# Kernel optimization log

Measured on AMD Instinct MI355X. Metric: run time of the kernel, lower is better.

## Reference

```python
import jax, jax.numpy as jnp
import numpy as np
from jax import lax

D = 256      # key/query dim
D_F = 256    # diff feature channels
C_TOK = 1    # leading context tokens in query_vit
EPS = 1e-6


def conv2d(x, w, b, pad):
    out = lax.conv_general_dilated(x, w, (1, 1), [(pad, pad), (pad, pad)],
                                   dimension_numbers=('NCHW', 'OIHW', 'NCHW'))
    return out + b[None, :, None, None]


def gn1(x, g, b):
    # GroupNorm with 1 group: normalize over (C,H,W) per sample
    mu = jnp.mean(x, axis=(1, 2, 3), keepdims=True)
    var = jnp.var(x, axis=(1, 2, 3), keepdims=True)
    xn = (x - mu) * lax.rsqrt(var + EPS)
    return xn * g[None, :, None, None] + b[None, :, None, None]


def resize_bilinear_ac(x, Ho, Wo):
    # F.interpolate(mode='bilinear', align_corners=True)
    B, C, H, W = x.shape
    ys = jnp.linspace(0.0, H - 1.0, Ho)
    xs = jnp.linspace(0.0, W - 1.0, Wo)
    y0 = jnp.floor(ys).astype(jnp.int32)
    y1 = jnp.minimum(y0 + 1, H - 1)
    wy = (ys - y0)[None, None, :, None]
    x0 = jnp.floor(xs).astype(jnp.int32)
    x1 = jnp.minimum(x0 + 1, W - 1)
    wx = (xs - x0)[None, None, None, :]
    r = x[:, :, y0, :] * (1.0 - wy) + x[:, :, y1, :] * wy
    return r[:, :, :, x0] * (1.0 - wx) + r[:, :, :, x1] * wx


def setup_inputs() -> dict:
    key = jax.random.key(0)
    ks = jax.random.split(key, 12)
    B, Hd, Wd, Ht, Wt = 8, 64, 64, 32, 32

    def kaiming(k, shape, fan_in):
        return jax.random.normal(k, shape, jnp.float32) * np.sqrt(2.0 / fan_in)

    return {
        'query_vit': jax.random.normal(ks[0], (B, C_TOK + Ht * Wt, D), jnp.float32),
        'feat_diff_cat': jax.random.normal(ks[1], (B, 5 * D_F, Hd, Wd), jnp.float32),
        'rb_w1': kaiming(ks[2], (D_F, 5 * D_F, 3, 3), 5 * D_F * 9), 'rb_b1': jnp.zeros((D_F,), jnp.float32),
        'rb_w2': kaiming(ks[3], (D_F, D_F, 3, 3), D_F * 9), 'rb_b2': jnp.zeros((D_F,), jnp.float32),
        'rb_ws': kaiming(ks[4], (D_F, 5 * D_F, 1, 1), 5 * D_F), 'rb_bs': jnp.zeros((D_F,), jnp.float32),
        'ln_g': jnp.ones((D_F,), jnp.float32), 'ln_b': jnp.zeros((D_F,), jnp.float32),
        'key_w': kaiming(ks[5], (D, D_F, 1, 1), D_F), 'key_b': jnp.zeros((D,), jnp.float32),
        'val_w': kaiming(ks[6], (D_F, D_F, 1, 1), D_F), 'val_b': jnp.zeros((D_F,), jnp.float32),
        'dh0_w': kaiming(ks[7], (D_F, D_F, 3, 3), D_F * 9), 'dh0_b': jnp.zeros((D_F,), jnp.float32),
        'dh1_w': kaiming(ks[8], (D_F, D_F, 3, 3), D_F * 9), 'dh1_b': jnp.zeros((D_F,), jnp.float32),
    }


def reference(query_vit, feat_diff_cat, rb_w1, rb_b1, rb_w2, rb_b2, rb_ws, rb_bs,
              ln_g, ln_b, key_w, key_b, val_w, val_b, dh0_w, dh0_b, dh1_w, dh1_b):
    B, _, h_diff, w_diff = feat_diff_cat.shape
    N = query_vit.shape[1] - C_TOK
    h_trm = w_trm = int(N ** 0.5)

    # ResBlock_ysh(D_f*5 -> D_f): conv3x3 + relu + conv3x3, 1x1-projected residual
    h = jax.nn.relu(conv2d(feat_diff_cat, rb_w1, rb_b1, 1))
    h = conv2d(h, rb_w2, rb_b2, 1)
    feat_diff = jax.nn.relu(h + conv2d(feat_diff_cat, rb_ws, rb_bs, 0))

    fln = gn1(feat_diff, ln_g, ln_b)
    key_diff = conv2d(fln, key_w, key_b, 0).reshape(B, D, -1)          # (B, D, HW)
    value_diff = conv2d(fln, val_w, val_b, 0).reshape(B, D_F, -1)      # (B, Df, HW)
    value_diff = jnp.transpose(value_diff, (0, 2, 1))                  # (B, HW, Df)

    # cross attention: (B, C+N, D) @ (B, D, HW) -> softmax -> @ (B, HW, Df)
    scores = jnp.einsum('bnd,bdm->bnm', query_vit, key_diff) * (D ** -0.5)
    attn = jax.nn.softmax(scores, axis=-1)
    out_cross = jnp.einsum('bnm,bmf->bnf', attn, value_diff)           # (B, C+N, Df)

    out_cross_c = out_cross[:, :C_TOK, :]
    out_p = jnp.transpose(out_cross[:, C_TOK:, :], (0, 2, 1)).reshape(B, D_F, h_trm, w_trm)
    out_p = jax.nn.relu(conv2d(out_p, dh0_w, dh0_b, 1))
    out_p = resize_bilinear_ac(out_p, h_diff, w_diff)
    out_p = out_p + feat_diff                                          # DropPath(0) = identity
    out_p = jax.nn.relu(conv2d(gn1(out_p, ln_g, ln_b), dh1_w, dh1_b, 1)) + out_p
    return out_cross_c, out_p
```

## Files before the change

kernel.cpp:

```cpp
#include <hip/hip_runtime.h>
#include <cstdint>
#include <cstddef>

typedef __attribute__((ext_vector_type(4))) float     f32x4;
typedef __attribute__((ext_vector_type(8))) __bf16    bf16x8;
typedef __attribute__((ext_vector_type(8))) short     short8;
typedef __attribute__((ext_vector_type(4))) unsigned short u16x4;
typedef unsigned short u16;

__device__ __forceinline__ float b2f(u16 u) {
  unsigned x = ((unsigned)u) << 16;
  float f;
  __builtin_memcpy(&f, &x, 4);
  return f;
}
__device__ __forceinline__ u16 f2b(float f) {
  unsigned u;
  __builtin_memcpy(&u, &f, 4);
  return (u16)((u + 0x7FFFu + ((u >> 16) & 1u)) >> 16);
}

struct GP {
  const u16*  A;
  const u16*  B;
  const float* bias;
  const void* aux;
  void*       C;
  float*      out0;
  long long   aBS, bBS, cBS, auxBS;
  int Ktot, Mrows, ldc;
  int cin, logW, wpad, poff;
  float scale;
};

#define GLDS16(g, l)                                                        \
  __builtin_amdgcn_global_load_lds(                                         \
      (const void __attribute__((address_space(1)))*)(g),                   \
      (void __attribute__((address_space(3)))*)(l), 16, 0, 0)

struct G256 {
  const u16* A;
  const u16* B;
  float* P;
  long long aBS;
  int Ktot, cin, logW, wpad, poff;
};

__global__ __launch_bounds__(512, 2) void k_gemm256(G256 gp) {
  const int tid = threadIdx.x;
  const int l = tid & 63, w = tid >> 6;
  const int lr = l & 15, lc = l >> 4;
  const int mt = blockIdx.x, sp = blockIdx.y, b = blockIdx.z;
  const int m0 = mt << 8;
  const int wm = w >> 2, wn = w & 3;

  __shared__ __align__(16) u16 sm[2][32768];
  u16* smb = &sm[0][0];

  f32x4 acc[8][4];
#pragma unroll
  for (int i = 0; i < 8; ++i)
#pragma unroll
    for (int j = 0; j < 4; ++j) acc[i][j] = (f32x4){0.f, 0.f, 0.f, 0.f};

  const u16* Ab = gp.A + (size_t)b * gp.aBS;
  const int slot = l & 3;
  const u16* aS[2];
  const u16* bS[2];
#pragma unroll
  for (int j = 0; j < 2; ++j) {
    const int r = j * 128 + w * 16 + (l >> 2);
    const int p = m0 + r;
    const int y = p >> gp.logW, x = p & ((1 << gp.logW) - 1);
    const int sw = (slot ^ ((r >> 1) & 3)) << 3;
    aS[j] = Ab + (size_t)((y + gp.poff) * gp.wpad + (x + gp.poff)) * gp.cin + sw;
    bS[j] = gp.B + (size_t)r * gp.Ktot + sw;
  }
  auto dstA = [&](int buf, int ks, int j) -> u16* {
    return smb + buf * 32768 + ks * 8192 + (j * 128 + w * 16) * 32 + l * 8;
  };
  auto dstB = [&](int buf, int ks, int j) -> u16* {
    return smb + buf * 32768 + 16384 + ks * 8192 + (j * 128 + w * 16) * 32 + l * 8;
  };

  const int Thalf = (gp.Ktot >> 6) >> 1;
  const int kt0 = sp * Thalf;
  int off = kt0 << 6;
  int tap = off / gp.cin;
  int kcS = off - tap * gp.cin;
  int dxS = tap % 3;
  int tapS = (tap / 3) * gp.wpad + dxS;
  int ktS = kt0;

  auto adv = [&](int& kA, int& kB) {
    kB = ktS << 6;
    kA = tapS * gp.cin + kcS;
    kcS += 64;
    if (kcS == gp.cin) {
      kcS = 0; ++dxS; ++tapS;
      if (dxS == 3) { dxS = 0; tapS += gp.wpad - 3; }
    }
    ++ktS;
  };

  {
    int kA, kB;
    adv(kA, kB);
    GLDS16(aS[0] + kA, dstA(0, 0, 0));
    GLDS16(aS[1] + kA, dstA(0, 0, 1));
    GLDS16(bS[0] + kB, dstB(0, 0, 0));
    GLDS16(bS[1] + kB, dstB(0, 0, 1));
    GLDS16(aS[0] + kA + 32, dstA(0, 1, 0));
    GLDS16(aS[1] + kA + 32, dstA(0, 1, 1));
    GLDS16(bS[0] + kB + 32, dstB(0, 1, 0));
    GLDS16(bS[1] + kB + 32, dstB(0, 1, 1));
  }
  asm volatile("s_waitcnt vmcnt(0)" ::: "memory");
  __builtin_amdgcn_s_barrier();

  const int NT = Thalf;
  for (int t = 0; t < NT; ++t) {
    const int buf = t & 1;
    const char* base = (const char*)smb + buf * 65536;
    const bool pf = (t + 1 < NT);
    if (pf) {
      int kA, kB;
      adv(kA, kB);
      GLDS16(aS[0] + kA, dstA(buf ^ 1, 0, 0));
      GLDS16(aS[1] + kA, dstA(buf ^ 1, 0, 1));
      GLDS16(bS[0] + kB, dstB(buf ^ 1, 0, 0));
      GLDS16(bS[1] + kB, dstB(buf ^ 1, 0, 1));
      GLDS16(aS[0] + kA + 32, dstA(buf ^ 1, 1, 0));
      GLDS16(aS[1] + kA + 32, dstA(buf ^ 1, 1, 1));
      GLDS16(bS[0] + kB + 32, dstB(buf ^ 1, 1, 0));
      GLDS16(bS[1] + kB + 32, dstB(buf ^ 1, 1, 1));
    }
    bf16x8 bv0[4], bv1[4];
#pragma unroll
    for (int ni = 0; ni < 4; ++ni) {
      const int row = wn * 64 + ni * 16 + lr;
      const int sw = (lc ^ ((row >> 1) & 3)) << 4;
      bv0[ni] = *(const bf16x8*)(base + 32768 + row * 64 + sw);
      bv1[ni] = *(const bf16x8*)(base + 49152 + row * 64 + sw);
    }
#pragma unroll
    for (int mq = 0; mq < 2; ++mq) {
      bf16x8 a0[4], a1[4];
#pragma unroll
      for (int mi = 0; mi < 4; ++mi) {
        const int row = wm * 128 + (mq * 4 + mi) * 16 + lr;
        const int sw = (lc ^ ((row >> 1) & 3)) << 4;
        a0[mi] = *(const bf16x8*)(base + row * 64 + sw);
        a1[mi] = *(const bf16x8*)(base + 16384 + row * 64 + sw);
      }
#pragma unroll
      for (int mi = 0; mi < 4; ++mi)
#pragma unroll
        for (int ni = 0; ni < 4; ++ni)
          acc[mq * 4 + mi][ni] = __builtin_amdgcn_mfma_f32_16x16x32_bf16(
              a0[mi], bv0[ni], acc[mq * 4 + mi][ni], 0, 0, 0);
#pragma unroll
      for (int mi = 0; mi < 4; ++mi)
#pragma unroll
        for (int ni = 0; ni < 4; ++ni)
          acc[mq * 4 + mi][ni] = __builtin_amdgcn_mfma_f32_16x16x32_bf16(
              a1[mi], bv1[ni], acc[mq * 4 + mi][ni], 0, 0, 0);
    }
    asm volatile("s_waitcnt vmcnt(0)" ::: "memory");
    __builtin_amdgcn_s_barrier();
  }

  float* P = gp.P + ((size_t)sp * 128 + b * 16 + mt) * 65536;
#pragma unroll
  for (int mi = 0; mi < 8; ++mi)
#pragma unroll
    for (int ni = 0; ni < 4; ++ni) {
      const int ncol = wn * 64 + ni * 16 + lr;
      const int mloc = wm * 128 + mi * 16 + lc * 4;
#pragma unroll
      for (int r = 0; r < 4; ++r)
        P[(size_t)(mloc + r) * 256 + ncol] = acc[mi][ni][r];
    }
}

__global__ __launch_bounds__(256) void k_reduceH1(const float* __restrict__ P,
                                                  const float* __restrict__ bias,
                                                  u16* __restrict__ o) {
  const int i4 = blockIdx.x * 256 + threadIdx.x;
  const int flat = i4 << 2;
  const int n0 = flat & 255;
  const int mloc = (flat >> 8) & 255;
  const int gm = flat >> 16;
  const f32x4 a = *(const f32x4*)(P + (size_t)gm * 65536 + mloc * 256 + n0);
  const f32x4 c = *(const f32x4*)(P + (size_t)(128 + gm) * 65536 + mloc * 256 + n0);
  const f32x4 bb = *(const f32x4*)(bias + n0);
  const int batch = gm >> 4;
  const int mg = (gm & 15) * 256 + mloc;
  const int y = mg >> 6, x = mg & 63;
  u16x4 r;
#pragma unroll
  for (int k = 0; k < 4; ++k) r[k] = f2b(fmaxf(a[k] + c[k] + bb[k], 0.f));
  *(u16x4*)(o + ((size_t)batch * 4356 + (size_t)(y + 1) * 66 + x + 1) * 256 + n0) = r;
}

template <int AMODE, int CW, bool RELU>
__global__ __launch_bounds__(512, 2) void k_gemm8(GP gp) {
  const int tid = threadIdx.x;
  const int l = tid & 63, w = tid >> 6;
  const int b = blockIdx.z;
  const int m0 = blockIdx.x * 128;
  const int wm = w >> 2, wn = w & 3;
  const int lr = l & 15, lc = l >> 4;

  __shared__ __align__(16) u16 sm[2][24576];

  f32x4 acc[4][4];
#pragma unroll
  for (int i = 0; i < 4; ++i)
#pragma unroll
    for (int j = 0; j < 4; ++j) acc[i][j] = (f32x4){0.f, 0.f, 0.f, 0.f};

  const u16* Ab = gp.A + (size_t)b * gp.aBS;
  const u16* Bb = gp.B + (size_t)b * gp.bBS;
  const int scoff = (((tid & 7) ^ ((tid >> 3) & 7)) << 3);

  const u16* aP[2];
  const u16* bP[4];
#pragma unroll
  for (int i = 0; i < 2; ++i) {
    const int p = m0 + i * 64 + (tid >> 3);
    if (AMODE == 0) {
      const int pc = p < gp.Mrows ? p : gp.Mrows - 1;
      aP[i] = Ab + (size_t)pc * gp.Ktot + scoff;
    } else {
      const int y = p >> gp.logW, x = p & ((1 << gp.logW) - 1);
      aP[i] = Ab + (size_t)((y + gp.poff) * gp.wpad + (x + gp.poff)) * gp.cin +
              scoff;
    }
  }
#pragma unroll
  for (int i = 0; i < 4; ++i)
    bP[i] = Bb + (size_t)(i * 64 + (tid >> 3)) * gp.Ktot + scoff;

  const int NT = gp.Ktot >> 6;
  int kcS = 0, tapS = 0, dxS = 0, ktS = 0;

  auto adv = [&](int& kA, int& kB) {
    kB = ktS << 6;
    if (AMODE == 0) {
      kA = ktS << 6;
    } else {
      kA = tapS * gp.cin + kcS;
      kcS += 64;
      if (kcS == gp.cin) {
        kcS = 0; ++dxS; ++tapS;
        if (dxS == 3) { dxS = 0; tapS += gp.wpad - 3; }
      }
    }
    ++ktS;
  };

  {
    int kA, kB;
    adv(kA, kB);
    u16* sA = &sm[0][0] + (w << 9);
    u16* sB = &sm[0][8192] + (w << 9);
    GLDS16(aP[0] + kA, sA);
    GLDS16(aP[1] + kA, sA + 4096);
    GLDS16(bP[0] + kB, sB);
    GLDS16(bP[1] + kB, sB + 4096);
    GLDS16(bP[2] + kB, sB + 8192);
    GLDS16(bP[3] + kB, sB + 12288);
  }
  asm volatile("s_waitcnt vmcnt(0)" ::: "memory");
  __builtin_amdgcn_s_barrier();

  for (int t = 0; t < NT; ++t) {
    const int buf = t & 1;
    const u16* sAc = &sm[buf][0];
    const u16* sBc = &sm[buf][8192];
    const bool pf = (t + 1 < NT);
    if (pf) {
      int kA, kB;
      adv(kA, kB);
      u16* sA = &sm[buf ^ 1][0] + (w << 9);
      u16* sB = &sm[buf ^ 1][8192] + (w << 9);
      GLDS16(aP[0] + kA, sA);
      GLDS16(aP[1] + kA, sA + 4096);
      GLDS16(bP[0] + kB, sB);
      GLDS16(bP[1] + kB, sB + 4096);
      GLDS16(bP[2] + kB, sB + 8192);
      GLDS16(bP[3] + kB, sB + 12288);
    }
    bf16x8 av0[4], av1[4], bv0[4], bv1[4];
#pragma unroll
    for (int mi = 0; mi < 4; ++mi) {
      const int row = wm * 64 + mi * 16 + lr;
      av0[mi] = *(const bf16x8*)(sAc + row * 64 + (((0 + lc) ^ (row & 7)) << 3));
      av1[mi] = *(const bf16x8*)(sAc + row * 64 + (((4 + lc) ^ (row & 7)) << 3));
    }
#pragma unroll
    for (int ni = 0; ni < 4; ++ni) {
      const int row = wn * 64 + ni * 16 + lr;
      bv0[ni] = *(const bf16x8*)(sBc + row * 64 + (((0 + lc) ^ (row & 7)) << 3));
      bv1[ni] = *(const bf16x8*)(sBc + row * 64 + (((4 + lc) ^ (row & 7)) << 3));
    }
#pragma unroll
    for (int mi = 0; mi < 4; ++mi)
#pragma unroll
      for (int ni = 0; ni < 4; ++ni)
        acc[mi][ni] = __builtin_amdgcn_mfma_f32_16x16x32_bf16(
            av0[mi], bv0[ni], acc[mi][ni], 0, 0, 0);
#pragma unroll
    for (int mi = 0; mi < 4; ++mi)
#pragma unroll
      for (int ni = 0; ni < 4; ++ni)
        acc[mi][ni] = __builtin_amdgcn_mfma_f32_16x16x32_bf16(
            av1[mi], bv1[ni], acc[mi][ni], 0, 0, 0);
    asm volatile("s_waitcnt vmcnt(0)" ::: "memory");
    __builtin_amdgcn_s_barrier();
  }

#pragma unroll
  for (int mi = 0; mi < 4; ++mi) {
#pragma unroll
    for (int ni = 0; ni < 4; ++ni) {
      const int ncol = wn * 64 + ni * 16 + lr;
      const int mbase = m0 + wm * 64 + mi * 16 + lc * 4;
      const float bv_ = gp.bias ? gp.bias[ncol] : 0.f;
      if constexpr (CW == 0) {
#pragma unroll
        for (int r = 0; r < 4; ++r) {
          float v = acc[mi][ni][r] + bv_;
          if (RELU) v = fmaxf(v, 0.f);
          ((u16*)gp.C)[(size_t)b * gp.cBS + (size_t)(mbase + r) * 256 + ncol] =
              f2b(v);
        }
      } else if constexpr (CW == 1) {
#pragma unroll
        for (int r = 0; r < 4; ++r) {
          float v = acc[mi][ni][r] + bv_;
          if (RELU) v = fmaxf(v, 0.f);
          const int mrow = mbase + r;
          const int y = mrow >> 6, x = mrow & 63;
          ((u16*)gp.C)[(size_t)b * gp.cBS +
                       (size_t)((y + 1) * 66 + x + 1) * 256 + ncol] = f2b(v);
        }
      } else if constexpr (CW == 2) {
#pragma unroll
        for (int r = 0; r < 4; ++r) {
          const int mrow = mbase + r;
          const float s =
              b2f(((const u16*)gp.aux)[(size_t)b * gp.auxBS +
                                       (size_t)mrow * 256 + ncol]);
          float v = acc[mi][ni][r] + bv_ + s;
          v = fmaxf(v, 0.f);
          ((float*)gp.C)[(size_t)b * gp.cBS + (size_t)mrow * 256 + ncol] = v;
        }
      } else if constexpr (CW == 6) {
        float* Cf =
            (float*)gp.C + (size_t)b * gp.cBS + (size_t)ncol * 4096 + mbase;
        const float* mid = (const float*)gp.aux + (size_t)b * gp.auxBS;
        f32x4 o;
#pragma unroll
        for (int r = 0; r < 4; ++r) {
          float v = acc[mi][ni][r] + bv_;
          v = fmaxf(v, 0.f);
          o[r] = v + mid[(size_t)(mbase + r) * 256 + ncol];
        }
        *(f32x4*)Cf = o;
      }
    }
  }
}

template <int AMODE, int CW, bool RELU>
__global__ __launch_bounds__(256, 2) void k_gemm(GP gp) {
  const int tid = threadIdx.x;
  const int l = tid & 63, w = tid >> 6;
  const int b = blockIdx.z;
  const int m0 = blockIdx.x * 128, n0 = blockIdx.y * 128;
  const int wm = w >> 1, wn = w & 1;

  __shared__ __align__(16) u16 smA[128 * 64];
  __shared__ __align__(16) u16 smB[128 * 64];

  f32x4 acc[4][4];
#pragma unroll
  for (int i = 0; i < 4; ++i)
#pragma unroll
    for (int j = 0; j < 4; ++j) acc[i][j] = (f32x4){0.f, 0.f, 0.f, 0.f};

  const u16* Ab = gp.A + (size_t)b * gp.aBS;
  const u16* Bb = gp.B + (size_t)b * gp.bBS;

  const int scoff = (((l & 7) ^ (l >> 3)) << 3);

  const u16* aRow[4];
  const u16* bRow[4];
  u16* ldsA[4];
  u16* ldsB[4];
#pragma unroll
  for (int i = 0; i < 4; ++i) {
    const int r = w * 32 + i * 8 + (l >> 3);
    bRow[i] = Bb + (size_t)(n0 + r) * gp.Ktot + scoff;
    const int p = m0 + r;
    if (AMODE == 0) {
      const int pc = p < gp.Mrows ? p : gp.Mrows - 1;
      aRow[i] = Ab + (size_t)pc * gp.Ktot + scoff;
    } else {
      const int y = p >> gp.logW, x = p & ((1 << gp.logW) - 1);
      const int icoord = (y + gp.poff) * gp.wpad + (x + gp.poff);
      aRow[i] = Ab + (size_t)icoord * gp.cin + scoff;
    }
    ldsA[i] = smA + (w * 32 + i * 8) * 64;
    ldsB[i] = smB + (w * 32 + i * 8) * 64;
  }

  const int ktiles = gp.Ktot >> 6;
  int tap_off = 0, dx = 0, kc = 0;

  for (int kt = 0; kt < ktiles; ++kt) {
    int koffA;
    if (AMODE == 0)
      koffA = kt << 6;
    else
      koffA = tap_off * gp.cin + kc;
    const int koffB = kt << 6;
#pragma unroll
    for (int i = 0; i < 4; ++i) GLDS16(aRow[i] + koffA, ldsA[i]);
#pragma unroll
    for (int i = 0; i < 4; ++i) GLDS16(bRow[i] + koffB, ldsB[i]);

    if (AMODE == 1) {
      kc += 64;
      if (kc == gp.cin) {
        kc = 0;
        ++dx;
        ++tap_off;
        if (dx == 3) { dx = 0; tap_off += gp.wpad - 3; }
      }
    }

    __syncthreads();
#pragma unroll
    for (int ks = 0; ks < 2; ++ks) {
      bf16x8 av[4], bv[4];
      const int cc = (ks << 2) + (l >> 4);
#pragma unroll
      for (int mi = 0; mi < 4; ++mi) {
        const int row = wm * 64 + mi * 16 + (l & 15);
        av[mi] = *(const bf16x8*)((const char*)smA + (row << 7) +
                                  ((cc ^ (row & 7)) << 4));
      }
#pragma unroll
      for (int ni = 0; ni < 4; ++ni) {
        const int row = wn * 64 + ni * 16 + (l & 15);
        bv[ni] = *(const bf16x8*)((const char*)smB + (row << 7) +
                                  ((cc ^ (row & 7)) << 4));
      }
#pragma unroll
      for (int mi = 0; mi < 4; ++mi)
#pragma unroll
        for (int ni = 0; ni < 4; ++ni)
          acc[mi][ni] = __builtin_amdgcn_mfma_f32_16x16x32_bf16(
              av[mi], bv[ni], acc[mi][ni], 0, 0, 0);
    }
    __syncthreads();
  }

#pragma unroll
  for (int mi = 0; mi < 4; ++mi) {
#pragma unroll
    for (int ni = 0; ni < 4; ++ni) {
      const int ncol = n0 + wn * 64 + ni * 16 + (l & 15);
      const int mbase = m0 + wm * 64 + mi * 16 + ((l >> 4) << 2);
      const float bv_ = gp.bias ? gp.bias[ncol] : 0.f;

      if constexpr (CW == 3) {
        u16* Cu = (u16*)gp.C + (size_t)b * gp.cBS + (size_t)ncol * 4096 + mbase;
        u16x4 pk;
#pragma unroll
        for (int r = 0; r < 4; ++r) pk[r] = f2b(acc[mi][ni][r] + bv_);
        *(u16x4*)Cu = pk;
      } else if constexpr (CW == 7) {
        u16* base = (u16*)gp.C;
        if (ncol < 256) {
#pragma unroll
          for (int r = 0; r < 4; ++r)
            base[(size_t)b * 1048576 + (size_t)(mbase + r) * 256 + ncol] =
                f2b(acc[mi][ni][r] + bv_);
        } else {
          u16x4 pk;
#pragma unroll
          for (int r = 0; r < 4; ++r) pk[r] = f2b(acc[mi][ni][r] + bv_);
          *(u16x4*)(base + 8388608 + (size_t)b * 1048576 +
                    (size_t)(ncol - 256) * 4096 + mbase) = pk;
        }
      } else {
#pragma unroll
        for (int reg = 0; reg < 4; ++reg) {
          const int mrow = mbase + reg;
          if (mrow >= gp.Mrows) continue;
          float v = acc[mi][ni][reg] * gp.scale + bv_;
          if (RELU) v = v > 0.f ? v : 0.f;
          if constexpr (CW == 0) {
            ((u16*)gp.C)[(size_t)b * gp.cBS + (size_t)mrow * gp.ldc + ncol] =
                f2b(v);
          } else if constexpr (CW == 4) {
            if (mrow == 0) {
              gp.out0[(size_t)b * 256 + ncol] = v;
            } else {
              const int p = mrow - 1, y = p >> 5, x = p & 31;
              ((u16*)gp.C)[(size_t)b * gp.cBS +
                           (size_t)((y + 1) * 34 + (x + 1)) * 256 + ncol] =
                  f2b(v);
            }
          } else if constexpr (CW == 5) {
            ((float*)gp.C)[(size_t)b * gp.cBS + (size_t)mrow * 256 + ncol] = v;
          }
        }
      }
    }
  }
}


__global__ __launch_bounds__(256) void k_prep_x(const float* __restrict__ x,
                                                u16* __restrict__ o) {
  __shared__ float t[32][65];
  const int b = blockIdx.z, c0 = blockIdx.y << 5, y = blockIdx.x;
  const float* src = x + ((size_t)b * 1280 + c0) * 4096 + (size_t)y * 64;
#pragma unroll
  for (int i = 0; i < 8; ++i) {
    const int idx = threadIdx.x + (i << 8);
    const int c = idx >> 6, xx = idx & 63;
    t[c][xx] = src[(size_t)c * 4096 + xx];
  }
  __syncthreads();
  u16* dst = o + ((size_t)b * 4356 + (size_t)(y + 1) * 66 + 1) * 1280 + c0;
#pragma unroll
  for (int i = 0; i < 8; ++i) {
    const int idx = threadIdx.x + (i << 8);
    const int xx = idx >> 5, c = idx & 31;
    dst[(size_t)xx * 1280 + c] = f2b(t[c][xx]);
  }
}

__global__ __launch_bounds__(256) void k_zero_border(u16* __restrict__ p,
                                                     int P, int C) {
  const int per_img = (4 * P - 4) * C;
  const int total = 8 * per_img;
  for (int idx = blockIdx.x * 256 + threadIdx.x; idx < total;
       idx += gridDim.x * 256) {
    const int b = idx / per_img;
    const int r = idx % per_img;
    const int pix = r / C, c = r % C;
    int y, x;
    const int Pm = P - 1;
    if (pix < P) { y = 0; x = pix; }
    else if (pix < 2 * P) { y = Pm; x = pix - P; }
    else if (pix < 3 * P - 2) { y = pix - 2 * P + 1; x = 0; }
    else { y = pix - (3 * P - 2) + 1; x = Pm; }
    p[((size_t)b * P * P + (size_t)y * P + x) * C + c] = 0;
  }
}

__global__ __launch_bounds__(256) void k_prep_w3(const float* __restrict__ w,
                                                 u16* __restrict__ o, int cin,
                                                 int n) {
  for (int i = blockIdx.x * 256 + threadIdx.x; i < n; i += gridDim.x * 256) {
    const int ci = i % cin;
    const int r = i / cin;
    const int t = r % 9;
    const int co = r / 9;
    o[i] = f2b(w[((size_t)co * cin + ci) * 9 + t]);
  }
}

__global__ __launch_bounds__(256) void k_f2b(const float* __restrict__ x,
                                             u16* __restrict__ o, int n) {
  for (int i = blockIdx.x * 256 + threadIdx.x; i < n; i += gridDim.x * 256)
    o[i] = f2b(x[i]);
}

__global__ __launch_bounds__(256) void k_gn_stats(const float* __restrict__ x,
                                                  float* __restrict__ st) {
  const int b = blockIdx.y;
  const f32x4* xb = (const f32x4*)(x + (size_t)b * 1048576);
  float s = 0.f, s2 = 0.f;
  for (int i = blockIdx.x * 256 + threadIdx.x; i < 262144;
       i += gridDim.x * 256) {
    const f32x4 v = xb[i];
    s += v[0] + v[1] + v[2] + v[3];
    s2 += v[0] * v[0] + v[1] * v[1] + v[2] * v[2] + v[3] * v[3];
  }
#pragma unroll
  for (int o = 32; o; o >>= 1) {
    s += __shfl_down(s, o);
    s2 += __shfl_down(s2, o);
  }
  __shared__ float ls[4], ls2[4];
  const int w = threadIdx.x >> 6;
  if ((threadIdx.x & 63) == 0) { ls[w] = s; ls2[w] = s2; }
  __syncthreads();
  if (threadIdx.x == 0) {
    atomicAdd(&st[b * 2], ls[0] + ls[1] + ls[2] + ls[3]);
    atomicAdd(&st[b * 2 + 1], ls2[0] + ls2[1] + ls2[2] + ls2[3]);
  }
}

template <bool PAD>
__global__ __launch_bounds__(256) void k_gn_norm(const float* __restrict__ x,
                                                 const float* __restrict__ st,
                                                 const float* __restrict__ g,
                                                 const float* __restrict__ bb,
                                                 u16* __restrict__ o) {
  const int b = blockIdx.y;
  const float mu = st[b * 2] * (1.f / 1048576.f);
  const float var = st[b * 2 + 1] * (1.f / 1048576.f) - mu * mu;
  const float rs = rsqrtf(var + 1e-6f);
  const int i4 = blockIdx.x * 256 + threadIdx.x;
  const f32x4 v = ((const f32x4*)(x + (size_t)b * 1048576))[i4];
  const int flat = i4 << 2;
  const int c = flat & 255;
  const int p = flat >> 8;
  const f32x4 gv = *(const f32x4*)(g + c);
  const f32x4 bv = *(const f32x4*)(bb + c);
  u16x4 r;
#pragma unroll
  for (int k = 0; k < 4; ++k) r[k] = f2b((v[k] - mu) * rs * gv[k] + bv[k]);
  size_t oidx;
  if (PAD) {
    const int y = p >> 6, xx = p & 63;
    oidx = ((size_t)b * 4356 + (size_t)(y + 1) * 66 + xx + 1) * 256 + c;
  } else {
    oidx = ((size_t)b * 4096 + p) * 256 + c;
  }
  *(u16x4*)(o + oidx) = r;
}

__global__ __launch_bounds__(256) void k_softmax(u16* __restrict__ s) {
  const size_t row = blockIdx.x;
  u16* p = s + row * 4096;
  const int t = threadIdx.x;
  const short8 r0 = ((const short8*)p)[t];
  const short8 r1 = ((const short8*)p)[t + 256];
  float v[16];
#pragma unroll
  for (int i = 0; i < 8; ++i) {
    v[i] = b2f((u16)r0[i]);
    v[8 + i] = b2f((u16)r1[i]);
  }
  float m = v[0];
#pragma unroll
  for (int i = 1; i < 16; ++i) m = fmaxf(m, v[i]);
#pragma unroll
  for (int o = 32; o; o >>= 1) m = fmaxf(m, __shfl_xor(m, o));
  __shared__ float lm[4], lsum[4];
  const int w = t >> 6;
  if ((t & 63) == 0) lm[w] = m;
  __syncthreads();
  m = fmaxf(fmaxf(lm[0], lm[1]), fmaxf(lm[2], lm[3]));
  float sum = 0.f;
#pragma unroll
  for (int i = 0; i < 16; ++i) {
    v[i] = __expf(v[i] - m);
    sum += v[i];
  }
#pragma unroll
  for (int o = 32; o; o >>= 1) sum += __shfl_xor(sum, o);
  if ((t & 63) == 0) lsum[w] = sum;
  __syncthreads();
  sum = lsum[0] + lsum[1] + lsum[2] + lsum[3];
  const float inv = 1.f / sum;
  short8 o0, o1;
#pragma unroll
  for (int i = 0; i < 8; ++i) {
    o0[i] = (short)f2b(v[i] * inv);
    o1[i] = (short)f2b(v[8 + i] * inv);
  }
  ((short8*)p)[t] = o0;
  ((short8*)p)[t + 256] = o1;
}

__global__ __launch_bounds__(256) void k_resize_add(const float* __restrict__ d0,
                                                    const float* __restrict__ F,
                                                    float* __restrict__ mid) {
  const int i4 = blockIdx.x * 256 + threadIdx.x;
  const int flat = i4 << 2;
  const int c = flat & 255;
  const int p = (flat >> 8) & 4095;
  const int b = flat >> 20;
  const int y = p >> 6, x = p & 63;
  const float fy = y * (31.f / 63.f);
  const int y0 = (int)fy;
  const float wy = fy - y0;
  const int y1 = y0 + 1 > 31 ? 31 : y0 + 1;
  const float fx = x * (31.f / 63.f);
  const int x0 = (int)fx;
  const float wx = fx - x0;
  const int x1 = x0 + 1 > 31 ? 31 : x0 + 1;
  const float* db = d0 + (size_t)b * 262144;
  const f32x4 a = *(const f32x4*)(db + ((size_t)(y0 * 32 + x0) << 8) + c);
  const f32x4 bq = *(const f32x4*)(db + ((size_t)(y0 * 32 + x1) << 8) + c);
  const f32x4 cq = *(const f32x4*)(db + ((size_t)(y1 * 32 + x0) << 8) + c);
  const f32x4 dq = *(const f32x4*)(db + ((size_t)(y1 * 32 + x1) << 8) + c);
  f32x4 r = (a * (1.f - wx) + bq * wx) * (1.f - wy) +
            (cq * (1.f - wx) + dq * wx) * wy;
  r += *(const f32x4*)(F + (size_t)flat);
  *(f32x4*)(mid + (size_t)flat) = r;
}


extern "C" void kernel_launch(void* const* d_in, const int* in_sizes, int n_in,
                              void* d_out, int out_size, void* d_ws,
                              size_t ws_size, hipStream_t stream) {
  (void)in_sizes; (void)n_in; (void)out_size;

  const float* q   = (const float*)d_in[0];
  const float* xdc = (const float*)d_in[1];
  const float* w1  = (const float*)d_in[2];
  const float* b1  = (const float*)d_in[3];
  const float* w2  = (const float*)d_in[4];
  const float* b2  = (const float*)d_in[5];
  const float* wsc = (const float*)d_in[6];
  const float* bsc = (const float*)d_in[7];
  const float* lng = (const float*)d_in[8];
  const float* lnb = (const float*)d_in[9];
  const float* wk  = (const float*)d_in[10];
  const float* bk  = (const float*)d_in[11];
  const float* wv  = (const float*)d_in[12];
  const float* bv  = (const float*)d_in[13];
  const float* wd0 = (const float*)d_in[14];
  const float* bd0 = (const float*)d_in[15];
  const float* wd1 = (const float*)d_in[16];
  const float* bd1 = (const float*)d_in[17];

  char* ws = (char*)d_ws;
  size_t cur = 0;
  auto alloc = [&](size_t sz) {
    char* p = ws + cur;
    cur += sz;
    return p;
  };
  u16* XPAD = (u16*)alloc(89194496);
  u16* W1R  = (u16*)alloc(5898240);
  u16* W2R  = (u16*)alloc(1179648);
  u16* WSR  = (u16*)alloc(655360);
  u16* WKV  = (u16*)alloc(262144);
  float* BKV = (float*)alloc(2048);
  u16* WD0R = (u16*)alloc(1179648);
  u16* WD1R = (u16*)alloc(1179648);
  u16* SB   = (u16*)alloc(16777216);
  u16* H1   = (u16*)alloc(17842176);
  float* F  = (float*)alloc(33554432);
  u16* FLN  = (u16*)alloc(16777216);
  u16* KT   = (u16*)alloc(16777216);
  u16* V    = (u16*)alloc(16777216);
  u16* QB   = (u16*)alloc(4198400);
  u16* OCP  = (u16*)alloc(4734976);
  float* D0O = (float*)alloc(8388608);
  float* MID = (float*)alloc(33554432);
  u16* G2   = (u16*)alloc(17842176);
  float* ST = (float*)alloc(256);
  u16* SCORES = XPAD;
  float* PART = (float*)FLN;
  (void)V;

  if (ws_size < cur) return;

  float* out0 = (float*)d_out;
  float* out1 = (float*)d_out + 2048;

  hipMemsetAsync(ST, 0, 256, stream);
  hipMemcpyAsync(BKV, bk, 1024, hipMemcpyDeviceToDevice, stream);
  hipMemcpyAsync(BKV + 256, bv, 1024, hipMemcpyDeviceToDevice, stream);

  k_zero_border<<<2048, 256, 0, stream>>>(XPAD, 66, 1280);
  k_zero_border<<<1024, 256, 0, stream>>>(H1, 66, 256);
  k_zero_border<<<1024, 256, 0, stream>>>(G2, 66, 256);

  k_prep_x<<<dim3(64, 40, 8), 256, 0, stream>>>(xdc, XPAD);
  k_prep_w3<<<2048, 256, 0, stream>>>(w1, W1R, 1280, 2949120);
  k_prep_w3<<<1024, 256, 0, stream>>>(w2, W2R, 256, 589824);
  k_prep_w3<<<1024, 256, 0, stream>>>(wd0, WD0R, 256, 589824);
  k_prep_w3<<<1024, 256, 0, stream>>>(wd1, WD1R, 256, 589824);
  k_f2b<<<512, 256, 0, stream>>>(wsc, WSR, 327680);
  k_f2b<<<128, 256, 0, stream>>>(wk, WKV, 65536);
  k_f2b<<<128, 256, 0, stream>>>(wv, WKV + 65536, 65536);

  const dim3 g8(32, 1, 8);
  {
    GP g{};
    g.A = XPAD; g.B = WSR; g.bias = bsc; g.C = SB;
    g.aBS = 5575680; g.bBS = 0; g.cBS = 1048576;
    g.Ktot = 1280; g.Mrows = 4096; g.ldc = 256;
    g.cin = 1280; g.logW = 6; g.wpad = 66; g.poff = 1; g.scale = 1.f;
    k_gemm8<1, 0, false><<<g8, 512, 0, stream>>>(g);
  }
  {
    G256 g{};
    g.A = XPAD; g.B = W1R; g.P = PART;
    g.aBS = 5575680; g.Ktot = 11520;
    g.cin = 1280; g.logW = 6; g.wpad = 66; g.poff = 0;
    k_gemm256<<<dim3(16, 2, 8), 512, 0, stream>>>(g);
    k_reduceH1<<<8192, 256, 0, stream>>>(PART, b1, H1);
  }
  k_f2b<<<2048, 256, 0, stream>>>(q, QB, 2099200);
  k_zero_border<<<512, 256, 0, stream>>>(OCP, 34, 256);

  {
    GP g{};
    g.A = H1; g.B = W2R; g.bias = b2; g.C = F; g.aux = SB;
    g.aBS = 1115136; g.bBS = 0; g.cBS = 1048576; g.auxBS = 1048576;
    g.Ktot = 2304; g.Mrows = 4096; g.ldc = 256;
    g.cin = 256; g.logW = 6; g.wpad = 66; g.poff = 0; g.scale = 1.f;
    k_gemm8<1, 2, false><<<g8, 512, 0, stream>>>(g);
  }
  k_gn_stats<<<dim3(64, 8), 256, 0, stream>>>(F, ST);
  k_gn_norm<false><<<dim3(1024, 8), 256, 0, stream>>>(F, ST, lng, lnb, FLN);
  {
    GP g{};
    g.A = FLN; g.B = WKV; g.bias = BKV; g.C = KT;
    g.aBS = 1048576; g.bBS = 0; g.cBS = 0;
    g.Ktot = 256; g.Mrows = 4096; g.ldc = 256; g.scale = 1.f;
    k_gemm<0, 7, false><<<dim3(32, 4, 8), 256, 0, stream>>>(g);
  }
  {
    GP g{};
    g.A = QB; g.B = KT; g.bias = nullptr; g.C = SCORES;
    g.aBS = 262400; g.bBS = 1048576; g.cBS = 4198400;
    g.Ktot = 256; g.Mrows = 1025; g.ldc = 4096; g.scale = 0.0625f;
    k_gemm<0, 0, false><<<dim3(9, 32, 8), 256, 0, stream>>>(g);
  }
  k_softmax<<<8200, 256, 0, stream>>>(SCORES);
  {
    GP g{};
    g.A = SCORES; g.B = V; g.bias = nullptr; g.C = OCP; g.out0 = out0;
    g.aBS = 4198400; g.bBS = 1048576; g.cBS = 295936;
    g.Ktot = 4096; g.Mrows = 1025; g.ldc = 256; g.scale = 1.f;
    k_gemm<0, 4, false><<<dim3(9, 2, 8), 256, 0, stream>>>(g);
  }
  {
    GP g{};
    g.A = OCP; g.B = WD0R; g.bias = bd0; g.C = D0O;
    g.aBS = 295936; g.bBS = 0; g.cBS = 262144;
    g.Ktot = 2304; g.Mrows = 1024; g.ldc = 256;
    g.cin = 256; g.logW = 5; g.wpad = 34; g.poff = 0; g.scale = 1.f;
    k_gemm<1, 5, true><<<dim3(8, 2, 8), 256, 0, stream>>>(g);
  }
  k_resize_add<<<8192, 256, 0, stream>>>(D0O, F, MID);
  k_gn_stats<<<dim3(64, 8), 256, 0, stream>>>(MID, ST + 16);
  k_gn_norm<true><<<dim3(1024, 8), 256, 0, stream>>>(MID, ST + 16, lng, lnb, G2);
  {
    GP g{};
    g.A = G2; g.B = WD1R; g.bias = bd1; g.C = out1; g.aux = MID;
    g.aBS = 1115136; g.bBS = 0; g.cBS = 1048576; g.auxBS = 1048576;
    g.Ktot = 2304; g.Mrows = 4096; g.ldc = 256;
    g.cin = 256; g.logW = 6; g.wpad = 66; g.poff = 0; g.scale = 1.f;
    k_gemm8<1, 6, false><<<g8, 512, 0, stream>>>(g);
  }
}
```

Measured before the change: 730.7 us.

## Fuse shortcut conv into conv2 GEMM, fold GroupNorm into K/V weights, merge prep kernels

The 1x1 shortcut conv is concatenated along K into the second 3x3 conv GEMM, so one GEMM reads H1 and the padded input and writes F in both fp32 and bf16. That GEMM's epilogue also accumulates the GroupNorm statistics with atomics. The first GroupNorm is then folded into per-batch key/value weights and biases by a small kernel, which removes the separate stats, normalize and FLN passes. The query scale moves into the query conversion, the second GroupNorm's stats move into the resize-add kernel, and the border-zeroing and weight-prep launches are merged into single kernels. In exchange, statistics come from atomics with a single-pass variance, and the folded per-batch weights are quantized to bf16 after scaling, which can change accuracy.

```diff
diff --git a/kernel.cpp b/kernel.cpp
--- a/kernel.cpp
+++ b/kernel.cpp
@@ -27,7 +27,8 @@
   const void* aux;
   void*       C;
   float*      out0;
-  long long   aBS, bBS, cBS, auxBS;
+  float*      st;
+  long long   aBS, bBS, cBS, auxBS, biasBS;
   int Ktot, Mrows, ldc;
   int cin, logW, wpad, poff;
   float scale;
@@ -203,7 +204,7 @@
   *(u16x4*)(o + ((size_t)batch * 4356 + (size_t)(y + 1) * 66 + x + 1) * 256 + n0) = r;
 }
 
-template <int AMODE, int CW, bool RELU>
+template <int AMODE, int CW>
 __global__ __launch_bounds__(512, 2) void k_gemm8(GP gp) {
   const int tid = threadIdx.x;
   const int l = tid & 63, w = tid >> 6;
@@ -225,53 +226,52 @@
   const int scoff = (((tid & 7) ^ ((tid >> 3) & 7)) << 3);
 
   const u16* aP[2];
-  const u16* bP[4];
+  const u16* aP2[2];
 #pragma unroll
   for (int i = 0; i < 2; ++i) {
     const int p = m0 + i * 64 + (tid >> 3);
-    if (AMODE == 0) {
-      const int pc = p < gp.Mrows ? p : gp.Mrows - 1;
-      aP[i] = Ab + (size_t)pc * gp.Ktot + scoff;
-    } else {
-      const int y = p >> gp.logW, x = p & ((1 << gp.logW) - 1);
-      aP[i] = Ab + (size_t)((y + gp.poff) * gp.wpad + (x + gp.poff)) * gp.cin +
-              scoff;
-    }
-  }
+    const int y = p >> 6, x = p & 63;
+    aP[i] = Ab + (size_t)(y * 66 + x) * gp.cin + scoff;
+    if (AMODE == 2) {
+      const u16* Xb = (const u16*)gp.aux + (size_t)b * gp.auxBS;
+      aP2[i] = Xb + (size_t)((y + 1) * 66 + (x + 1)) * 1280 + scoff;
+    }
+  }
+  const u16* bP[4];
 #pragma unroll
   for (int i = 0; i < 4; ++i)
     bP[i] = Bb + (size_t)(i * 64 + (tid >> 3)) * gp.Ktot + scoff;
 
   const int NT = gp.Ktot >> 6;
-  int kcS = 0, tapS = 0, dxS = 0, ktS = 0;
-
-  auto adv = [&](int& kA, int& kB) {
-    kB = ktS << 6;
-    if (AMODE == 0) {
-      kA = ktS << 6;
+  const int seg1t = (AMODE == 2) ? 36 : 0x7fffffff;
+  int kcS = 0, tapS = 0, dxS = 0, nstg = 0;
+
+  auto stage = [&](int buf) {
+    const int kt = nstg++;
+    const int kB = kt << 6;
+    u16* sA = &sm[buf][0] + (w << 9);
+    u16* sB = &sm[buf][8192] + (w << 9);
+    if (AMODE == 2 && kt >= seg1t) {
+      const int kA = (kt - seg1t) << 6;
+      GLDS16(aP2[0] + kA, sA);
+      GLDS16(aP2[1] + kA, sA + 4096);
     } else {
-      kA = tapS * gp.cin + kcS;
+      const int kA = tapS * gp.cin + kcS;
       kcS += 64;
       if (kcS == gp.cin) {
         kcS = 0; ++dxS; ++tapS;
-        if (dxS == 3) { dxS = 0; tapS += gp.wpad - 3; }
+        if (dxS == 3) { dxS = 0; tapS += 63; }
       }
-    }
-    ++ktS;
-  };
-
-  {
-    int kA, kB;
-    adv(kA, kB);
-    u16* sA = &sm[0][0] + (w << 9);
-    u16* sB = &sm[0][8192] + (w << 9);
-    GLDS16(aP[0] + kA, sA);
-    GLDS16(aP[1] + kA, sA + 4096);
+      GLDS16(aP[0] + kA, sA);
+      GLDS16(aP[1] + kA, sA + 4096);
+    }
     GLDS16(bP[0] + kB, sB);
     GLDS16(bP[1] + kB, sB + 4096);
     GLDS16(bP[2] + kB, sB + 8192);
     GLDS16(bP[3] + kB, sB + 12288);
-  }
+  };
+
+  stage(0);
   asm volatile("s_waitcnt vmcnt(0)" ::: "memory");
   __builtin_amdgcn_s_barrier();
 
@@ -279,19 +279,8 @@
     const int buf = t & 1;
     const u16* sAc = &sm[buf][0];
     const u16* sBc = &sm[buf][8192];
-    const bool pf = (t + 1 < NT);
-    if (pf) {
-      int kA, kB;
-      adv(kA, kB);
-      u16* sA = &sm[buf ^ 1][0] + (w << 9);
-      u16* sB = &sm[buf ^ 1][8192] + (w << 9);
-      GLDS16(aP[0] + kA, sA);
-      GLDS16(aP[1] + kA, sA + 4096);
-      GLDS16(bP[0] + kB, sB);
-      GLDS16(bP[1] + kB, sB + 4096);
-      GLDS16(bP[2] + kB, sB + 8192);
-      GLDS16(bP[3] + kB, sB + 12288);
-    }
+    if (t + 1 < NT) stage(buf ^ 1);
+
     bf16x8 av0[4], av1[4], bv0[4], bv1[4];
 #pragma unroll
     for (int mi = 0; mi < 4; ++mi) {
@@ -321,55 +310,56 @@
     __builtin_amdgcn_s_barrier();
   }
 
+  float lsum = 0.f, lsq = 0.f;
 #pragma unroll
   for (int mi = 0; mi < 4; ++mi) {
 #pragma unroll
     for (int ni = 0; ni < 4; ++ni) {
       const int ncol = wn * 64 + ni * 16 + lr;
       const int mbase = m0 + wm * 64 + mi * 16 + lc * 4;
-      const float bv_ = gp.bias ? gp.bias[ncol] : 0.f;
-      if constexpr (CW == 0) {
+      const float bv_ = gp.bias[ncol];
+      if constexpr (CW == 8) {
+        float* F = (float*)gp.C + (size_t)b * gp.cBS;
+        u16* FB = (u16*)gp.out0 + (size_t)b * gp.cBS;
 #pragma unroll
         for (int r = 0; r < 4; ++r) {
-          float v = acc[mi][ni][r] + bv_;
-          if (RELU) v = fmaxf(v, 0.f);
-          ((u16*)gp.C)[(size_t)b * gp.cBS + (size_t)(mbase + r) * 256 + ncol] =
-              f2b(v);
+          float v = fmaxf(acc[mi][ni][r] + bv_, 0.f);
+          const size_t idx = (size_t)(mbase + r) * 256 + ncol;
+          F[idx] = v;
+          FB[idx] = f2b(v);
+          lsum += v;
+          lsq += v * v;
         }
-      } else if constexpr (CW == 1) {
-#pragma unroll
-        for (int r = 0; r < 4; ++r) {
-          float v = acc[mi][ni][r] + bv_;
-          if (RELU) v = fmaxf(v, 0.f);
-          const int mrow = mbase + r;
-          const int y = mrow >> 6, x = mrow & 63;
-          ((u16*)gp.C)[(size_t)b * gp.cBS +
-                       (size_t)((y + 1) * 66 + x + 1) * 256 + ncol] = f2b(v);
-        }
-      } else if constexpr (CW == 2) {
-#pragma unroll
-        for (int r = 0; r < 4; ++r) {
-          const int mrow = mbase + r;
-          const float s =
-              b2f(((const u16*)gp.aux)[(size_t)b * gp.auxBS +
-                                       (size_t)mrow * 256 + ncol]);
-          float v = acc[mi][ni][r] + bv_ + s;
-          v = fmaxf(v, 0.f);
-          ((float*)gp.C)[(size_t)b * gp.cBS + (size_t)mrow * 256 + ncol] = v;
-        }
-      } else if constexpr (CW == 6) {
+      } else {
         float* Cf =
             (float*)gp.C + (size_t)b * gp.cBS + (size_t)ncol * 4096 + mbase;
         const float* mid = (const float*)gp.aux + (size_t)b * gp.auxBS;
         f32x4 o;
 #pragma unroll
         for (int r = 0; r < 4; ++r) {
-          float v = acc[mi][ni][r] + bv_;
-          v = fmaxf(v, 0.f);
+          float v = fmaxf(acc[mi][ni][r] + bv_, 0.f);
           o[r] = v + mid[(size_t)(mbase + r) * 256 + ncol];
         }
         *(f32x4*)Cf = o;
       }
+    }
+  }
+  if constexpr (CW == 8) {
+    __syncthreads();
+#pragma unroll
+    for (int o = 32; o; o >>= 1) {
+      lsum += __shfl_down(lsum, o);
+      lsq += __shfl_down(lsq, o);
+    }
+    float* red = (float*)&sm[0][0];
+    if (l == 0) { red[w * 2] = lsum; red[w * 2 + 1] = lsq; }
+    __syncthreads();
+    if (tid == 0) {
+      float s = 0.f, s2 = 0.f;
+#pragma unroll
+      for (int k = 0; k < 8; ++k) { s += red[k * 2]; s2 += red[k * 2 + 1]; }
+      atomicAdd(&gp.st[b * 2], s);
+      atomicAdd(&gp.st[b * 2 + 1], s2);
     }
   }
 }
@@ -475,15 +465,10 @@
     for (int ni = 0; ni < 4; ++ni) {
       const int ncol = n0 + wn * 64 + ni * 16 + (l & 15);
       const int mbase = m0 + wm * 64 + mi * 16 + ((l >> 4) << 2);
-      const float bv_ = gp.bias ? gp.bias[ncol] : 0.f;
-
-      if constexpr (CW == 3) {
-        u16* Cu = (u16*)gp.C + (size_t)b * gp.cBS + (size_t)ncol * 4096 + mbase;
-        u16x4 pk;
-#pragma unroll
-        for (int r = 0; r < 4; ++r) pk[r] = f2b(acc[mi][ni][r] + bv_);
-        *(u16x4*)Cu = pk;
-      } else if constexpr (CW == 7) {
+      const float bv_ =
+          gp.bias ? gp.bias[(size_t)b * gp.biasBS + ncol] : 0.f;
+
+      if constexpr (CW == 7) {
         u16* base = (u16*)gp.C;
         if (ncol < 256) {
 #pragma unroll
@@ -547,67 +532,98 @@
   }
 }
 
-__global__ __launch_bounds__(256) void k_zero_border(u16* __restrict__ p,
-                                                     int P, int C) {
+__device__ __forceinline__ void zb1(u16* p, int P, int C, int idx) {
   const int per_img = (4 * P - 4) * C;
-  const int total = 8 * per_img;
-  for (int idx = blockIdx.x * 256 + threadIdx.x; idx < total;
-       idx += gridDim.x * 256) {
-    const int b = idx / per_img;
-    const int r = idx % per_img;
-    const int pix = r / C, c = r % C;
-    int y, x;
-    const int Pm = P - 1;
-    if (pix < P) { y = 0; x = pix; }
-    else if (pix < 2 * P) { y = Pm; x = pix - P; }
-    else if (pix < 3 * P - 2) { y = pix - 2 * P + 1; x = 0; }
-    else { y = pix - (3 * P - 2) + 1; x = Pm; }
-    p[((size_t)b * P * P + (size_t)y * P + x) * C + c] = 0;
-  }
-}
-
-__global__ __launch_bounds__(256) void k_prep_w3(const float* __restrict__ w,
-                                                 u16* __restrict__ o, int cin,
-                                                 int n) {
-  for (int i = blockIdx.x * 256 + threadIdx.x; i < n; i += gridDim.x * 256) {
-    const int ci = i % cin;
-    const int r = i / cin;
-    const int t = r % 9;
-    const int co = r / 9;
-    o[i] = f2b(w[((size_t)co * cin + ci) * 9 + t]);
-  }
-}
-
-__global__ __launch_bounds__(256) void k_f2b(const float* __restrict__ x,
-                                             u16* __restrict__ o, int n) {
-  for (int i = blockIdx.x * 256 + threadIdx.x; i < n; i += gridDim.x * 256)
-    o[i] = f2b(x[i]);
-}
-
-__global__ __launch_bounds__(256) void k_gn_stats(const float* __restrict__ x,
-                                                  float* __restrict__ st) {
-  const int b = blockIdx.y;
-  const f32x4* xb = (const f32x4*)(x + (size_t)b * 1048576);
-  float s = 0.f, s2 = 0.f;
-  for (int i = blockIdx.x * 256 + threadIdx.x; i < 262144;
+  const int b = idx / per_img;
+  const int r = idx % per_img;
+  const int pix = r / C, c = r % C;
+  int y, x;
+  const int Pm = P - 1;
+  if (pix < P) { y = 0; x = pix; }
+  else if (pix < 2 * P) { y = Pm; x = pix - P; }
+  else if (pix < 3 * P - 2) { y = pix - 2 * P + 1; x = 0; }
+  else { y = pix - (3 * P - 2) + 1; x = Pm; }
+  p[((size_t)b * P * P + (size_t)y * P + x) * C + c] = 0;
+}
+
+__global__ __launch_bounds__(256) void k_zero_borders(u16* XPAD, u16* H1,
+                                                      u16* G2, u16* OCP) {
+  const int nx = 8 * 260 * 1280;
+  const int nh = 8 * 260 * 256;
+  const int no = 8 * 132 * 256;
+  const int total = nx + 2 * nh + no;
+  for (int i = blockIdx.x * 256 + threadIdx.x; i < total;
        i += gridDim.x * 256) {
-    const f32x4 v = xb[i];
-    s += v[0] + v[1] + v[2] + v[3];
-    s2 += v[0] * v[0] + v[1] * v[1] + v[2] * v[2] + v[3] * v[3];
-  }
-#pragma unroll
-  for (int o = 32; o; o >>= 1) {
-    s += __shfl_down(s, o);
-    s2 += __shfl_down(s2, o);
-  }
-  __shared__ float ls[4], ls2[4];
-  const int w = threadIdx.x >> 6;
-  if ((threadIdx.x & 63) == 0) { ls[w] = s; ls2[w] = s2; }
-  __syncthreads();
-  if (threadIdx.x == 0) {
-    atomicAdd(&st[b * 2], ls[0] + ls[1] + ls[2] + ls[3]);
-    atomicAdd(&st[b * 2 + 1], ls2[0] + ls2[1] + ls2[2] + ls2[3]);
-  }
+    if (i < nx) zb1(XPAD, 66, 1280, i);
+    else if (i < nx + nh) zb1(H1, 66, 256, i - nx);
+    else if (i < nx + 2 * nh) zb1(G2, 66, 256, i - nx - nh);
+    else zb1(OCP, 34, 256, i - nx - 2 * nh);
+  }
+}
+
+__global__ __launch_bounds__(256) void k_prep_all(
+    const float* __restrict__ w1, const float* __restrict__ w2,
+    const float* __restrict__ wsc, const float* __restrict__ wd0,
+    const float* __restrict__ wd1, const float* __restrict__ b2,
+    const float* __restrict__ bsc, const float* __restrict__ q,
+    u16* __restrict__ W1R, u16* __restrict__ WCAT2, u16* __restrict__ WD0R,
+    u16* __restrict__ WD1R, float* __restrict__ BB2, u16* __restrict__ QB) {
+  const int N1 = 2949120, N2 = 917504, N3 = 589824, N4 = 589824,
+            N5 = 2099200, N6 = 256;
+  const int T = N1 + N2 + N3 + N4 + N5 + N6;
+  for (int i = blockIdx.x * 256 + threadIdx.x; i < T; i += gridDim.x * 256) {
+    if (i < N1) {
+      const int ci = i % 1280, r = i / 1280, t = r % 9, co = r / 9;
+      W1R[i] = f2b(w1[((size_t)co * 1280 + ci) * 9 + t]);
+    } else if (i < N1 + N2) {
+      const int k = i - N1;
+      const int co = k / 3584, kk = k % 3584;
+      float v;
+      if (kk < 2304) {
+        const int tap = kk / 256, ci = kk % 256;
+        v = w2[((size_t)co * 256 + ci) * 9 + tap];
+      } else {
+        v = wsc[(size_t)co * 1280 + (kk - 2304)];
+      }
+      WCAT2[k] = f2b(v);
+    } else if (i < N1 + N2 + N3) {
+      const int k = i - N1 - N2;
+      const int ci = k % 256, r = k / 256, t = r % 9, co = r / 9;
+      WD0R[k] = f2b(wd0[((size_t)co * 256 + ci) * 9 + t]);
+    } else if (i < N1 + N2 + N3 + N4) {
+      const int k = i - N1 - N2 - N3;
+      const int ci = k % 256, r = k / 256, t = r % 9, co = r / 9;
+      WD1R[k] = f2b(wd1[((size_t)co * 256 + ci) * 9 + t]);
+    } else if (i < N1 + N2 + N3 + N4 + N5) {
+      const int k = i - N1 - N2 - N3 - N4;
+      QB[k] = f2b(q[k] * 0.0625f);
+    } else {
+      const int k = i - N1 - N2 - N3 - N4 - N5;
+      BB2[k] = b2[k] + bsc[k];
+    }
+  }
+}
+
+__global__ __launch_bounds__(256) void k_foldkv(
+    const float* __restrict__ wk, const float* __restrict__ wv,
+    const float* __restrict__ bk, const float* __restrict__ bv,
+    const float* __restrict__ g, const float* __restrict__ lnb,
+    const float* __restrict__ st, u16* __restrict__ WKVB,
+    float* __restrict__ BKVB) {
+  const int idx = blockIdx.x * 256 + threadIdx.x;
+  const int b = idx >> 9, j = idx & 511;
+  const float mu = st[b * 2] * (1.f / 1048576.f);
+  const float var = st[b * 2 + 1] * (1.f / 1048576.f) - mu * mu;
+  const float rs = rsqrtf(var + 1e-6f);
+  const float* wrow = (j < 256) ? wk + (size_t)j * 256 : wv + (size_t)(j - 256) * 256;
+  float acc = (j < 256) ? bk[j] : bv[j - 256];
+  u16* orow = WKVB + ((size_t)b * 512 + j) * 256;
+  for (int c = 0; c < 256; ++c) {
+    const float wv_ = wrow[c];
+    orow[c] = f2b(wv_ * g[c] * rs);
+    acc += wv_ * (lnb[c] - mu * rs * g[c]);
+  }
+  BKVB[b * 512 + j] = acc;
 }
 
 template <bool PAD>
@@ -686,7 +702,8 @@
 
 __global__ __launch_bounds__(256) void k_resize_add(const float* __restrict__ d0,
                                                     const float* __restrict__ F,
-                                                    float* __restrict__ mid) {
+                                                    float* __restrict__ mid,
+                                                    float* __restrict__ st) {
   const int i4 = blockIdx.x * 256 + threadIdx.x;
   const int flat = i4 << 2;
   const int c = flat & 255;
@@ -710,6 +727,23 @@
             (cq * (1.f - wx) + dq * wx) * wy;
   r += *(const f32x4*)(F + (size_t)flat);
   *(f32x4*)(mid + (size_t)flat) = r;
+
+  float ls = r[0] + r[1] + r[2] + r[3];
+  float lq = r[0] * r[0] + r[1] * r[1] + r[2] * r[2] + r[3] * r[3];
+#pragma unroll
+  for (int o = 32; o; o >>= 1) {
+    ls += __shfl_down(ls, o);
+    lq += __shfl_down(lq, o);
+  }
+  __shared__ float red[8];
+  const int w = threadIdx.x >> 6;
+  if ((threadIdx.x & 63) == 0) { red[w * 2] = ls; red[w * 2 + 1] = lq; }
+  __syncthreads();
+  if (threadIdx.x == 0) {
+    const int bb = blockIdx.x >> 10;
+    atomicAdd(&st[16 + bb * 2], red[0] + red[2] + red[4] + red[6]);
+    atomicAdd(&st[16 + bb * 2 + 1], red[1] + red[3] + red[5] + red[7]);
+  }
 }
 
 
@@ -744,28 +778,27 @@
     cur += sz;
     return p;
   };
-  u16* XPAD = (u16*)alloc(89194496);
-  u16* W1R  = (u16*)alloc(5898240);
-  u16* W2R  = (u16*)alloc(1179648);
-  u16* WSR  = (u16*)alloc(655360);
-  u16* WKV  = (u16*)alloc(262144);
-  float* BKV = (float*)alloc(2048);
-  u16* WD0R = (u16*)alloc(1179648);
-  u16* WD1R = (u16*)alloc(1179648);
-  u16* SB   = (u16*)alloc(16777216);
-  u16* H1   = (u16*)alloc(17842176);
-  float* F  = (float*)alloc(33554432);
-  u16* FLN  = (u16*)alloc(16777216);
-  u16* KT   = (u16*)alloc(16777216);
-  u16* V    = (u16*)alloc(16777216);
-  u16* QB   = (u16*)alloc(4198400);
-  u16* OCP  = (u16*)alloc(4734976);
+  u16* XPAD  = (u16*)alloc(89194496);
+  u16* W1R   = (u16*)alloc(5898240);
+  u16* WCAT2 = (u16*)alloc(1835008);
+  u16* WD0R  = (u16*)alloc(1179648);
+  u16* WD1R  = (u16*)alloc(1179648);
+  u16* WKVB  = (u16*)alloc(2097152);
+  float* BKVB = (float*)alloc(16384);
+  float* BB2 = (float*)alloc(1024);
+  u16* H1    = (u16*)alloc(17842176);
+  float* F   = (float*)alloc(33554432);
+  u16* FB    = (u16*)alloc(16777216);
+  u16* KT    = (u16*)alloc(16777216);
+  u16* V     = (u16*)alloc(16777216);
+  u16* QB    = (u16*)alloc(4198400);
+  u16* OCP   = (u16*)alloc(4734976);
   float* D0O = (float*)alloc(8388608);
   float* MID = (float*)alloc(33554432);
-  u16* G2   = (u16*)alloc(17842176);
-  float* ST = (float*)alloc(256);
+  u16* G2    = (u16*)alloc(17842176);
+  float* ST  = (float*)alloc(256);
   u16* SCORES = XPAD;
-  float* PART = (float*)FLN;
+  float* PART = (float*)F;
   (void)V;
 
   if (ws_size < cur) return;
@@ -774,31 +807,11 @@
   float* out1 = (float*)d_out + 2048;
 
   hipMemsetAsync(ST, 0, 256, stream);
-  hipMemcpyAsync(BKV, bk, 1024, hipMemcpyDeviceToDevice, stream);
-  hipMemcpyAsync(BKV + 256, bv, 1024, hipMemcpyDeviceToDevice, stream);
-
-  k_zero_border<<<2048, 256, 0, stream>>>(XPAD, 66, 1280);
-  k_zero_border<<<1024, 256, 0, stream>>>(H1, 66, 256);
-  k_zero_border<<<1024, 256, 0, stream>>>(G2, 66, 256);
-
+  k_zero_borders<<<2048, 256, 0, stream>>>(XPAD, H1, G2, OCP);
   k_prep_x<<<dim3(64, 40, 8), 256, 0, stream>>>(xdc, XPAD);
-  k_prep_w3<<<2048, 256, 0, stream>>>(w1, W1R, 1280, 2949120);
-  k_prep_w3<<<1024, 256, 0, stream>>>(w2, W2R, 256, 589824);
-  k_prep_w3<<<1024, 256, 0, stream>>>(wd0, WD0R, 256, 589824);
-  k_prep_w3<<<1024, 256, 0, stream>>>(wd1, WD1R, 256, 589824);
-  k_f2b<<<512, 256, 0, stream>>>(wsc, WSR, 327680);
-  k_f2b<<<128, 256, 0, stream>>>(wk, WKV, 65536);
-  k_f2b<<<128, 256, 0, stream>>>(wv, WKV + 65536, 65536);
-
-  const dim3 g8(32, 1, 8);
-  {
-    GP g{};
-    g.A = XPAD; g.B = WSR; g.bias = bsc; g.C = SB;
-    g.aBS = 5575680; g.bBS = 0; g.cBS = 1048576;
-    g.Ktot = 1280; g.Mrows = 4096; g.ldc = 256;
-    g.cin = 1280; g.logW = 6; g.wpad = 66; g.poff = 1; g.scale = 1.f;
-    k_gemm8<1, 0, false><<<g8, 512, 0, stream>>>(g);
-  }
+  k_prep_all<<<4096, 256, 0, stream>>>(w1, w2, wsc, wd0, wd1, b2, bsc, q, W1R,
+                                       WCAT2, WD0R, WD1R, BB2, QB);
+
   {
     G256 g{};
     g.A = XPAD; g.B = W1R; g.P = PART;
@@ -807,23 +820,20 @@
     k_gemm256<<<dim3(16, 2, 8), 512, 0, stream>>>(g);
     k_reduceH1<<<8192, 256, 0, stream>>>(PART, b1, H1);
   }
-  k_f2b<<<2048, 256, 0, stream>>>(q, QB, 2099200);
-  k_zero_border<<<512, 256, 0, stream>>>(OCP, 34, 256);
-
   {
     GP g{};
-    g.A = H1; g.B = W2R; g.bias = b2; g.C = F; g.aux = SB;
-    g.aBS = 1115136; g.bBS = 0; g.cBS = 1048576; g.auxBS = 1048576;
-    g.Ktot = 2304; g.Mrows = 4096; g.ldc = 256;
+    g.A = H1; g.B = WCAT2; g.bias = BB2; g.aux = XPAD; g.C = F;
+    g.out0 = (float*)FB; g.st = ST;
+    g.aBS = 1115136; g.bBS = 0; g.cBS = 1048576; g.auxBS = 5575680;
+    g.Ktot = 3584; g.Mrows = 4096; g.ldc = 256;
     g.cin = 256; g.logW = 6; g.wpad = 66; g.poff = 0; g.scale = 1.f;
-    k_gemm8<1, 2, false><<<g8, 512, 0, stream>>>(g);
-  }
-  k_gn_stats<<<dim3(64, 8), 256, 0, stream>>>(F, ST);
-  k_gn_norm<false><<<dim3(1024, 8), 256, 0, stream>>>(F, ST, lng, lnb, FLN);
+    k_gemm8<2, 8><<<dim3(32, 1, 8), 512, 0, stream>>>(g);
+  }
+  k_foldkv<<<16, 256, 0, stream>>>(wk, wv, bk, bv, lng, lnb, ST, WKVB, BKVB);
   {
     GP g{};
-    g.A = FLN; g.B = WKV; g.bias = BKV; g.C = KT;
-    g.aBS = 1048576; g.bBS = 0; g.cBS = 0;
+    g.A = FB; g.B = WKVB; g.bias = BKVB; g.C = KT;
+    g.aBS = 1048576; g.bBS = 131072; g.cBS = 0; g.biasBS = 512;
     g.Ktot = 256; g.Mrows = 4096; g.ldc = 256; g.scale = 1.f;
     k_gemm<0, 7, false><<<dim3(32, 4, 8), 256, 0, stream>>>(g);
   }
@@ -831,7 +841,7 @@
     GP g{};
     g.A = QB; g.B = KT; g.bias = nullptr; g.C = SCORES;
     g.aBS = 262400; g.bBS = 1048576; g.cBS = 4198400;
-    g.Ktot = 256; g.Mrows = 1025; g.ldc = 4096; g.scale = 0.0625f;
+    g.Ktot = 256; g.Mrows = 1025; g.ldc = 4096; g.scale = 1.f;
     k_gemm<0, 0, false><<<dim3(9, 32, 8), 256, 0, stream>>>(g);
   }
   k_softmax<<<8200, 256, 0, stream>>>(SCORES);
@@ -845,13 +855,12 @@
   {
     GP g{};
     g.A = OCP; g.B = WD0R; g.bias = bd0; g.C = D0O;
-    g.aBS = 295936; g.bBS = 0; g.cBS = 262144;
+    g.aBS = 295936; g.bBS = 0; g.cBS = 262144; g.biasBS = 0;
     g.Ktot = 2304; g.Mrows = 1024; g.ldc = 256;
     g.cin = 256; g.logW = 5; g.wpad = 34; g.poff = 0; g.scale = 1.f;
     k_gemm<1, 5, true><<<dim3(8, 2, 8), 256, 0, stream>>>(g);
   }
-  k_resize_add<<<8192, 256, 0, stream>>>(D0O, F, MID);
-  k_gn_stats<<<dim3(64, 8), 256, 0, stream>>>(MID, ST + 16);
+  k_resize_add<<<8192, 256, 0, stream>>>(D0O, F, MID, ST);
   k_gn_norm<true><<<dim3(1024, 8), 256, 0, stream>>>(MID, ST + 16, lng, lnb, G2);
   {
     GP g{};
@@ -859,6 +868,6 @@
     g.aBS = 1115136; g.bBS = 0; g.cBS = 1048576; g.auxBS = 1048576;
     g.Ktot = 2304; g.Mrows = 4096; g.ldc = 256;
     g.cin = 256; g.logW = 6; g.wpad = 66; g.poff = 0; g.scale = 1.f;
-    k_gemm8<1, 6, false><<<g8, 512, 0, stream>>>(g);
-  }
-}
+    k_gemm8<1, 6><<<dim3(32, 1, 8), 512, 0, stream>>>(g);
+  }
+}
```

After: 886.1 us. +21.3%, slower.
